# Optimization experiments

Hardware: AMD Instinct MI355X
Metric: run time of the kernel (lower is better)

Reference implementation:

```python
import jax, jax.numpy as jnp
import numpy as np

DN = ('NCHW', 'OIHW', 'NCHW')

def conv(x, w, b, stride, pad):
    y = jax.lax.conv_general_dilated(x, w, (stride, stride), ((pad, pad), (pad, pad)), dimension_numbers=DN)
    return y + b[None, :, None, None]

def conv_transpose(x, w, b, stride, pad):
    # w has torch ConvTranspose2d layout (Cin, Cout, kh, kw)
    k = w.shape[2]
    w_f = jnp.transpose(w[:, :, ::-1, ::-1], (1, 0, 2, 3))  # -> OIHW, spatially flipped
    p = k - 1 - pad
    y = jax.lax.conv_general_dilated(x, w_f, (1, 1), ((p, p), (p, p)), lhs_dilation=(stride, stride), dimension_numbers=DN)
    return y + b[None, :, None, None]

def setup_inputs() -> dict:
    key = jax.random.key(0)
    ks = jax.random.split(key, 16)
    K, D = 512, 64
    s = 0.05
    inp = {
        'x': jax.random.uniform(ks[0], (32, 3, 256, 256), dtype=jnp.float32),
        'enc_w1': jax.random.normal(ks[1], (32, 3, 4, 4), jnp.float32) * s,
        'enc_b1': jnp.zeros((32,), jnp.float32),
        'enc_w2': jax.random.normal(ks[2], (64, 32, 4, 4), jnp.float32) * s,
        'enc_b2': jnp.zeros((64,), jnp.float32),
        'enc_w3': jax.random.normal(ks[3], (D, 64, 3, 3), jnp.float32) * s,
        'enc_b3': jnp.zeros((D,), jnp.float32),
        'codebook': jax.random.uniform(ks[4], (K, D), jnp.float32, -1.0 / K, 1.0 / K),
        'dec_w1': jax.random.normal(ks[5], (D, 64, 4, 4), jnp.float32) * s,   # ConvT (Cin,Cout,k,k)
        'dec_b1': jnp.zeros((64,), jnp.float32),
        'dec_w2': jax.random.normal(ks[6], (64, 32, 4, 4), jnp.float32) * s,  # ConvT
        'dec_b2': jnp.zeros((32,), jnp.float32),
        'dec_w3': jax.random.normal(ks[7], (3, 32, 3, 3), jnp.float32) * s,
        'dec_b3': jnp.zeros((3,), jnp.float32),
    }
    return inp

COMMITMENT_COST = 0.25

def reference(x, enc_w1, enc_b1, enc_w2, enc_b2, enc_w3, enc_b3, codebook,
              dec_w1, dec_b1, dec_w2, dec_b2, dec_w3, dec_b3):
    sg = jax.lax.stop_gradient
    # encoder
    h = jax.nn.relu(conv(x, enc_w1, enc_b1, 2, 1))
    h = jax.nn.relu(conv(h, enc_w2, enc_b2, 2, 1))
    z = conv(h, enc_w3, enc_b3, 1, 1)  # [B, D, H/4, W/4]
    # vector quantizer
    D = codebook.shape[1]
    z_perm = jnp.transpose(z, (0, 2, 3, 1))  # BHWD
    flat = z_perm.reshape(-1, D)  # [N, D]
    dist = jnp.sum(flat * flat, axis=1, keepdims=True) - 2.0 * (flat @ codebook.T) + jnp.sum(codebook * codebook, axis=1)  # [N, K]
    idx = jnp.argmin(dist, axis=1)
    q = codebook[idx].reshape(z_perm.shape)
    q = jnp.transpose(q, (0, 3, 1, 2))  # BDHW
    vq_loss = jnp.mean((sg(q) - z) ** 2) + COMMITMENT_COST * jnp.mean((q - sg(z)) ** 2)
    q_st = z + sg(q - z)  # straight-through
    # decoder
    h = jax.nn.relu(conv_transpose(q_st, dec_w1, dec_b1, 2, 1))
    h = jax.nn.relu(conv_transpose(h, dec_w2, dec_b2, 2, 1))
    recon = jax.nn.sigmoid(conv(h, dec_w3, dec_b3, 1, 1))
    return recon, vq_loss
```

## Files before the change

kernel.cpp:

```cpp
#include <hip/hip_runtime.h>

typedef unsigned short u16;
typedef unsigned int u32;
typedef __attribute__((ext_vector_type(8))) short bf16x8;
typedef __attribute__((ext_vector_type(4))) float f32x4;

#define MFMA(a, b, c) __builtin_amdgcn_mfma_f32_16x16x32_bf16(a, b, c, 0, 0, 0)

__device__ __forceinline__ float b2f(u32 lo16) {
  union { u32 i; float f; } v; v.i = lo16 << 16; return v.f;
}
__device__ __forceinline__ u16 f2b(float f) {
  union { float f; u32 i; } v; v.f = f;
  return (u16)((v.i + 0x7fffu + ((v.i >> 16) & 1u)) >> 16);
}
__device__ __forceinline__ u16 f2bt(float f) {
  union { float f; u32 i; } v; v.f = f;
  return (u16)(v.i >> 16);
}
__device__ __forceinline__ bf16x8 ld8(const u16* p) { return *(const bf16x8*)p; }

__global__ void prep_k(const float* __restrict__ ew1, const float* __restrict__ ew2,
                       const float* __restrict__ ew3, const float* __restrict__ dw1,
                       const float* __restrict__ dw2, const float* __restrict__ dw3,
                       const float* __restrict__ cb,
                       float* W1, u16* Bp2, u16* Bp3, u16* BpT1, u16* BpT2,
                       u16* Bpd3, u16* Bpvq, float* cnorm, float* loss) {
  int tid = blockIdx.x * blockDim.x + threadIdx.x;
  int nth = gridDim.x * blockDim.x;
  for (int i = tid; i < 1536; i += nth) {
    int oc = i & 31; int r = i >> 5; int kw = r & 3; r >>= 2; int kh = r & 3; int ic = r >> 2;
    W1[i] = ew1[((oc*3 + ic)*4 + kh)*4 + kw];
  }
  for (int i = tid; i < 32768; i += nth) {
    int j = i & 7, li = (i >> 3) & 63, nt = (i >> 9) & 3, t = i >> 11;
    int ic = 8*(li >> 4) + j, oc = 16*nt + (li & 15), kh = t >> 2, kw = t & 3;
    Bp2[i] = f2b(ew2[((oc*32 + ic)*4 + kh)*4 + kw]);
  }
  for (int i = tid; i < 36864; i += nth) {
    int j = i & 7, li = (i >> 3) & 63, nt = (i >> 9) & 3, kc = (i >> 11) & 1, t = i >> 12;
    int ic = 32*kc + 8*(li >> 4) + j, oc = 16*nt + (li & 15), kh = t / 3, kw = t % 3;
    Bp3[i] = f2b(ew3[((oc*64 + ic)*3 + kh)*3 + kw]);
  }
  for (int i = tid; i < 65536; i += nth) {
    int j = i & 7, li = (i >> 3) & 63, nt = (i >> 9) & 3, kc = (i >> 11) & 1,
        t = (i >> 12) & 3, p = i >> 14;
    int a = p >> 1, b = p & 1;
    int ky = (1 - a) + 2*(t >> 1), kx = (1 - b) + 2*(t & 1);
    int ic = 32*kc + 8*(li >> 4) + j, oc = 16*nt + (li & 15);
    BpT1[i] = f2b(dw1[((ic*64 + oc)*4 + ky)*4 + kx]);
  }
  for (int i = tid; i < 32768; i += nth) {
    int j = i & 7, li = (i >> 3) & 63, nt = (i >> 9) & 1, kc = (i >> 10) & 1,
        t = (i >> 11) & 3, p = i >> 13;
    int a = p >> 1, b = p & 1;
    int ky = (1 - a) + 2*(t >> 1), kx = (1 - b) + 2*(t & 1);
    int ic = 32*kc + 8*(li >> 4) + j, oc = 16*nt + (li & 15);
    BpT2[i] = f2b(dw2[((ic*32 + oc)*4 + ky)*4 + kx]);
  }
  for (int i = tid; i < 4608; i += nth) {
    int j = i & 7, li = (i >> 3) & 63, t = i >> 9;
    int n = li & 15, ic = 8*(li >> 4) + j, kh = t / 3, kw = t % 3;
    Bpd3[i] = (n < 3) ? f2b(dw3[((n*32 + ic)*3 + kh)*3 + kw]) : (u16)0;
  }
  for (int i = tid; i < 32768; i += nth) {
    int j = i & 7, li = (i >> 3) & 63, nt = (i >> 9) & 31, kc = i >> 14;
    int d = 32*kc + 8*(li >> 4) + j, code = 16*nt + (li & 15);
    Bpvq[i] = f2b(cb[code*64 + d]);
  }
  for (int k = tid; k < 512; k += nth) {
    float s = 0.f;
    for (int d = 0; d < 64; ++d) { float c = cb[k*64 + d]; s += c*c; }
    cnorm[k] = s;
  }
  if (tid == 0) *loss = 0.f;
}

__global__ __launch_bounds__(256) void conv1_k(
    const float* __restrict__ x, const float* __restrict__ W1,
    const float* __restrict__ b1, u16* __restrict__ h1) {
  __shared__ float ins[3*18*36];
  int Tx = blockIdx.x, Ty = blockIdx.y, b = blockIdx.z;
  int tid = threadIdx.x;
  for (int i = tid; i < 3*18*36; i += 256) {
    int c = i % 36; int r = (i / 36) % 18; int ic = i / 648;
    int iy = 16*Ty - 1 + r, ix = 32*Tx - 2 + c;
    float v = 0.f;
    if ((unsigned)iy < 256u && (unsigned)ix < 256u)
      v = x[((size_t)(b*3 + ic)*256 + iy)*256 + ix];
    ins[i] = v;
  }
  __syncthreads();
  int posg = tid & 31, ocg = tid >> 5;
  int Y = posg >> 2, Xg = posg & 3;
  int oc0 = ocg * 4;
  float acc[4][4];
#pragma unroll
  for (int j = 0; j < 4; ++j) { float bv = b1[oc0 + j];
#pragma unroll
    for (int e = 0; e < 4; ++e) acc[j][e] = bv; }
  for (int ic = 0; ic < 3; ++ic)
#pragma unroll
    for (int kh = 0; kh < 4; ++kh) {
      const float* row = &ins[ic*648 + (2*Y + kh)*36 + 8*Xg];
      float win[12];
#pragma unroll
      for (int t = 0; t < 12; ++t) win[t] = row[t];
#pragma unroll
      for (int kw = 0; kw < 4; ++kw) {
        const float* wp = &W1[((ic*4 + kh)*4 + kw)*32 + oc0];
        float w0 = wp[0], w1 = wp[1], w2 = wp[2], w3 = wp[3];
#pragma unroll
        for (int e = 0; e < 4; ++e) {
          float v = win[2*e + kw + 1];
          acc[0][e] += w0*v; acc[1][e] += w1*v; acc[2][e] += w2*v; acc[3][e] += w3*v;
        }
      }
    }
  int oy = 8*Ty + Y;
  int oxb = 16*Tx + 4*Xg;
#pragma unroll
  for (int e = 0; e < 4; ++e) {
    u16* op = &h1[((size_t)(b*128 + oy)*128 + oxb + e)*32 + oc0];
#pragma unroll
    for (int j = 0; j < 4; ++j) op[j] = f2b(fmaxf(acc[j][e], 0.f));
  }
}

__global__ __launch_bounds__(256) void conv2_k(
    const u16* __restrict__ h1, const u16* __restrict__ Bp2,
    const float* __restrict__ eb2, u16* __restrict__ h2) {
  __shared__ u16 lds[2448*8];
  int Tx = blockIdx.x, Ty = blockIdx.y, img = blockIdx.z;
  int tid = threadIdx.x;
  for (int i = tid; i < 2448; i += 256) {
    int c = i & 3; int x = (i >> 2) % 34; int row = (i >> 2) / 34;
    int iy = 16*Ty - 1 + row, ix = 32*Tx - 1 + x;
    f32x4 v = {0,0,0,0};
    if ((unsigned)iy < 128u && (unsigned)ix < 128u)
      v = *(const f32x4*)(h1 + (((size_t)(img*128 + iy)*128 + ix)*32 + c*8));
    *(f32x4*)(lds + ((row*4 + c)*34 + x)*8) = v;
  }
  __syncthreads();
  int w = tid >> 6, l = tid & 63, lg = l >> 4, lc = l & 15;
  f32x4 acc[2][4];
#pragma unroll
  for (int nt = 0; nt < 4; ++nt) {
    float bv = eb2[nt*16 + lc];
    acc[0][nt] = (f32x4){bv,bv,bv,bv}; acc[1][nt] = (f32x4){bv,bv,bv,bv};
  }
#pragma unroll
  for (int t = 0; t < 16; ++t) {
    int kh = t >> 2, kw = t & 3;
    bf16x8 a0 = ld8(lds + (((2*w + kh)*4 + lg)*34 + 2*lc + kw)*8);
    bf16x8 a1 = ld8(lds + (((2*(w+4) + kh)*4 + lg)*34 + 2*lc + kw)*8);
    const u16* bp = Bp2 + t*2048 + l*8;
    bf16x8 b0 = ld8(bp), b1 = ld8(bp + 512), b2v = ld8(bp + 1024), b3v = ld8(bp + 1536);
    acc[0][0] = MFMA(a0, b0, acc[0][0]); acc[0][1] = MFMA(a0, b1, acc[0][1]);
    acc[0][2] = MFMA(a0, b2v, acc[0][2]); acc[0][3] = MFMA(a0, b3v, acc[0][3]);
    acc[1][0] = MFMA(a1, b0, acc[1][0]); acc[1][1] = MFMA(a1, b1, acc[1][1]);
    acc[1][2] = MFMA(a1, b2v, acc[1][2]); acc[1][3] = MFMA(a1, b3v, acc[1][3]);
  }
#pragma unroll
  for (int m = 0; m < 2; ++m) {
    int oy = 8*Ty + w + m*4;
#pragma unroll
    for (int nt = 0; nt < 4; ++nt)
#pragma unroll
      for (int r = 0; r < 4; ++r) {
        int e = 4*lg + r;
        h2[((size_t)(img*64 + oy)*64 + 16*Tx + e)*64 + nt*16 + lc] =
            f2b(fmaxf(acc[m][nt][r], 0.f));
      }
  }
}

__global__ __launch_bounds__(256) void conv3e_k(
    const u16* __restrict__ h2, const u16* __restrict__ Bp3,
    const float* __restrict__ eb3, u16* __restrict__ z) {
  __shared__ u16 lds[1440*8];
  int Tx = blockIdx.x, Ty = blockIdx.y, img = blockIdx.z;
  int tid = threadIdx.x;
  for (int i = tid; i < 1440; i += 256) {
    int c = i & 7; int x = (i >> 3) % 18; int row = (i >> 3) / 18;
    int iy = 8*Ty - 1 + row, ix = 16*Tx - 1 + x;
    f32x4 v = {0,0,0,0};
    if ((unsigned)iy < 64u && (unsigned)ix < 64u)
      v = *(const f32x4*)(h2 + (((size_t)(img*64 + iy)*64 + ix)*64 + c*8));
    *(f32x4*)(lds + ((row*8 + c)*18 + x)*8) = v;
  }
  __syncthreads();
  int w = tid >> 6, l = tid & 63, lg = l >> 4, lc = l & 15;
  f32x4 acc[2][4];
#pragma unroll
  for (int nt = 0; nt < 4; ++nt) {
    float bv = eb3[nt*16 + lc];
    acc[0][nt] = (f32x4){bv,bv,bv,bv}; acc[1][nt] = (f32x4){bv,bv,bv,bv};
  }
#pragma unroll
  for (int t = 0; t < 9; ++t) {
    int kh = t / 3, kw = t % 3;
#pragma unroll
    for (int kc = 0; kc < 2; ++kc) {
      bf16x8 a0 = ld8(lds + (((w + kh)*8 + kc*4 + lg)*18 + lc + kw)*8);
      bf16x8 a1 = ld8(lds + (((w + 4 + kh)*8 + kc*4 + lg)*18 + lc + kw)*8);
      const u16* bp = Bp3 + (t*2 + kc)*2048 + l*8;
      bf16x8 b0 = ld8(bp), b1 = ld8(bp + 512), b2v = ld8(bp + 1024), b3v = ld8(bp + 1536);
      acc[0][0] = MFMA(a0, b0, acc[0][0]); acc[0][1] = MFMA(a0, b1, acc[0][1]);
      acc[0][2] = MFMA(a0, b2v, acc[0][2]); acc[0][3] = MFMA(a0, b3v, acc[0][3]);
      acc[1][0] = MFMA(a1, b0, acc[1][0]); acc[1][1] = MFMA(a1, b1, acc[1][1]);
      acc[1][2] = MFMA(a1, b2v, acc[1][2]); acc[1][3] = MFMA(a1, b3v, acc[1][3]);
    }
  }
#pragma unroll
  for (int m = 0; m < 2; ++m) {
    int oy = 8*Ty + w + m*4;
#pragma unroll
    for (int nt = 0; nt < 4; ++nt)
#pragma unroll
      for (int r = 0; r < 4; ++r) {
        int e = 4*lg + r;
        z[((size_t)(img*64 + oy)*64 + 16*Tx + e)*64 + nt*16 + lc] = f2b(acc[m][nt][r]);
      }
  }
}

__global__ __launch_bounds__(256) void vqm_k(
    const u16* __restrict__ z, const u16* __restrict__ Bpvq,
    const float* __restrict__ cnorm, const float* __restrict__ cbf,
    u16* __restrict__ q, float* __restrict__ loss) {
  __shared__ u16 cbl[32768];
  __shared__ float cnl[512];
  __shared__ int idxl[64];
  __shared__ float red[256];
  int tid = threadIdx.x;
  for (int i = tid; i < 4096; i += 256)
    *(f32x4*)(cbl + i*8) = *(const f32x4*)(Bpvq + i*8);
  for (int i = tid; i < 512; i += 256) cnl[i] = cnorm[i];
  __syncthreads();
  int w = tid >> 6, l = tid & 63, lg = l >> 4, lc = l & 15;
  int wglobal = blockIdx.x*4 + w;
  float lsum = 0.f;
  for (int it = 0; it < 8; ++it) {
    int mf = wglobal + it*1024;
    size_t P = (size_t)mf * 16;
    bf16x8 a0 = ld8(z + (P + lc)*64 + lg*8);
    bf16x8 a1 = ld8(z + (P + lc)*64 + 32 + lg*8);
    float best[4] = {1e30f, 1e30f, 1e30f, 1e30f};
    int bidx[4] = {0, 0, 0, 0};
    for (int nt = 0; nt < 32; ++nt) {
      f32x4 acc = {0,0,0,0};
      acc = MFMA(a0, ld8(cbl + (nt*64 + l)*8), acc);
      acc = MFMA(a1, ld8(cbl + ((32 + nt)*64 + l)*8), acc);
      float cn = cnl[nt*16 + lc];
      int code = nt*16 + lc;
#pragma unroll
      for (int r = 0; r < 4; ++r) {
        float dist = cn - 2.f*acc[r];
        if (dist < best[r]) { best[r] = dist; bidx[r] = code; }
      }
    }
#pragma unroll
    for (int r = 0; r < 4; ++r) {
      float b = best[r]; int bi = bidx[r];
      for (int m = 1; m < 16; m <<= 1) {
        float ob = __shfl_xor(b, m);
        int oi = __shfl_xor(bi, m);
        if (ob < b || (ob == b && oi < bi)) { b = ob; bi = oi; }
      }
      if (lc == 0) idxl[w*16 + lg*4 + r] = bi;
    }
    int m = lc, ch0 = lg*16;
    int id = idxl[w*16 + m];
    const float* crow = cbf + (size_t)id*64 + ch0;
    const u16* zp = z + (P + m)*64 + ch0;
    u32* qp = (u32*)(q + (P + m)*64 + ch0);
#pragma unroll
    for (int c = 0; c < 16; c += 2) {
      float c0 = crow[c], c1 = crow[c+1];
      float d0 = c0 - b2f(zp[c]), d1 = c1 - b2f(zp[c+1]);
      lsum += d0*d0 + d1*d1;
      qp[c >> 1] = (u32)f2bt(c0) | ((u32)f2bt(c1) << 16);
    }
  }
  red[tid] = lsum;
  __syncthreads();
  for (int s = 128; s > 0; s >>= 1) {
    if (tid < s) red[tid] += red[tid + s];
    __syncthreads();
  }
  if (tid == 0) atomicAdd(loss, red[0] * (1.25f / 8388608.f));
}

__global__ __launch_bounds__(256) void convt1_k(
    const u16* __restrict__ q, const u16* __restrict__ BpT1,
    const float* __restrict__ db1, u16* __restrict__ d1) {
  __shared__ u16 lds[864*8];
  int Tx = blockIdx.x, Ty = blockIdx.y, img = blockIdx.z;
  int X0 = 16*Tx, P0 = 4*Ty;
  int tid = threadIdx.x;
  for (int i = tid; i < 864; i += 256) {
    int c = i & 7; int x = (i >> 3) % 18; int row = (i >> 3) / 18;
    int iy = P0 - 1 + row, ix = X0 - 1 + x;
    f32x4 v = {0,0,0,0};
    if ((unsigned)iy < 64u && (unsigned)ix < 64u)
      v = *(const f32x4*)(q + (((size_t)(img*64 + iy)*64 + ix)*64 + c*8));
    *(f32x4*)(lds + ((row*8 + c)*18 + x)*8) = v;
  }
  __syncthreads();
  int w = tid >> 6, l = tid & 63, lg = l >> 4, lc = l & 15;
  int a = w & 1, bp_ = w >> 1;
  f32x4 acc[4][4];
#pragma unroll
  for (int nt = 0; nt < 4; ++nt) {
    float bv = db1[nt*16 + lc];
#pragma unroll
    for (int m = 0; m < 4; ++m) acc[m][nt] = (f32x4){bv,bv,bv,bv};
  }
  const u16* bbase = BpT1 + (size_t)(a*2 + bp_)*16384;
#pragma unroll
  for (int t = 0; t < 4; ++t) {
    int kyi = t >> 1, kxi = t & 1;
#pragma unroll
    for (int kc = 0; kc < 2; ++kc) {
      const u16* bp = bbase + (t*2 + kc)*2048 + l*8;
      bf16x8 b0 = ld8(bp), b1 = ld8(bp + 512), b2v = ld8(bp + 1024), b3v = ld8(bp + 1536);
      int xg = lc + bp_ - kxi + 1;
#pragma unroll
      for (int m = 0; m < 4; ++m) {
        int rowg = m + a - kyi + 1;
        bf16x8 av = ld8(lds + ((rowg*8 + kc*4 + lg)*18 + xg)*8);
        acc[m][0] = MFMA(av, b0, acc[m][0]);
        acc[m][1] = MFMA(av, b1, acc[m][1]);
        acc[m][2] = MFMA(av, b2v, acc[m][2]);
        acc[m][3] = MFMA(av, b3v, acc[m][3]);
      }
    }
  }
#pragma unroll
  for (int m = 0; m < 4; ++m) {
    int oy = 2*(P0 + m) + a;
#pragma unroll
    for (int nt = 0; nt < 4; ++nt)
#pragma unroll
      for (int r = 0; r < 4; ++r) {
        int e = 4*lg + r;
        int ox = 2*(X0 + e) + bp_;
        d1[((size_t)(img*128 + oy)*128 + ox)*64 + nt*16 + lc] =
            f2bt(fmaxf(acc[m][nt][r], 0.f));
      }
  }
}

__global__ __launch_bounds__(256) void tail_k(
    const u16* __restrict__ d1, const u16* __restrict__ BpT2,
    const float* __restrict__ db2, const u16* __restrict__ Bpd3,
    const float* __restrict__ db3, float* __restrict__ out) {
  __shared__ u16 d1s[680*8];
  __shared__ u16 d2q[8192];
  int Tx = blockIdx.x, Ty = blockIdx.y, img = blockIdx.z;
  int DX0 = 30*Tx - 1, DY0 = 6*Ty - 1;
  int IYB = 3*Ty, IXB = 15*Tx;
  int tid = threadIdx.x;
  for (int i = tid; i < 680; i += 256) {
    int x = i % 17; int rc = i / 17; int c = rc & 7; int row = rc >> 3;
    int iy = IYB - 1 + row, ix = IXB - 1 + x;
    f32x4 v = {0,0,0,0};
    if ((unsigned)iy < 128u && (unsigned)ix < 128u)
      v = *(const f32x4*)(d1 + (((size_t)(img*128 + iy)*128 + ix)*64 + c*8));
    *(f32x4*)(d1s + ((row*8 + c)*17 + x)*8) = v;
  }
  __syncthreads();
  int w = tid >> 6, l = tid & 63, lg = l >> 4, lc = l & 15;
  {
    int a = w & 1, b = w >> 1;
    f32x4 acc[4][2];
#pragma unroll
    for (int nt = 0; nt < 2; ++nt) {
      float bv = db2[nt*16 + lc];
#pragma unroll
      for (int m = 0; m < 4; ++m) acc[m][nt] = (f32x4){bv,bv,bv,bv};
    }
    const u16* bbase = BpT2 + (size_t)(a*2 + b)*8192;
#pragma unroll
    for (int kxi = 0; kxi < 2; ++kxi) {
      int xg = lc - kxi + 1;
#pragma unroll
      for (int kc = 0; kc < 2; ++kc) {
        bf16x8 av[5];
#pragma unroll
        for (int rr = 0; rr < 5; ++rr)
          av[rr] = ld8(d1s + ((rr*8 + kc*4 + lg)*17 + xg)*8);
#pragma unroll
        for (int kyi = 0; kyi < 2; ++kyi) {
          int t = kyi*2 + kxi;
          const u16* bb = bbase + (t*2 + kc)*1024 + l*8;
          bf16x8 b0 = ld8(bb), b1 = ld8(bb + 512);
#pragma unroll
          for (int m = 0; m < 4; ++m) {
            acc[m][0] = MFMA(av[m + 1 - kyi], b0, acc[m][0]);
            acc[m][1] = MFMA(av[m + 1 - kyi], b1, acc[m][1]);
          }
        }
      }
    }
    int oyb = DY0 + (1 - a);
    int oxb = DX0 + (1 - b) + 8*lg;
    bool cm[4];
#pragma unroll
    for (int r = 0; r < 4; ++r) cm[r] = (unsigned)(oxb + 2*r) < 256u;
    int base = (a*2 + b)*2048 + lg*128 + lc;
    int ntk = (lg & 1);
#pragma unroll
    for (int m = 0; m < 4; ++m) {
      bool rm = (unsigned)(oyb + 2*m) < 256u;
#pragma unroll
      for (int nt = 0; nt < 2; ++nt) {
        int wb = base + m*512 + ((nt ^ ntk) << 4);
#pragma unroll
        for (int r = 0; r < 4; ++r) {
          float v = (rm && cm[r]) ? fmaxf(acc[m][nt][r], 0.f) : 0.f;
          d2q[wb + r*32] = f2bt(v);
        }
      }
    }
  }
  __syncthreads();
  bf16x8 bw[9];
#pragma unroll
  for (int t = 0; t < 9; ++t) bw[t] = ld8(Bpd3 + t*512 + l*8);
  float bv3 = (lc < 3) ? db3[lc] : 0.f;
#pragma unroll
  for (int i = 0; i < 3; ++i) {
    int u = w + 4*i;
    int yy = u >> 1, xf = u & 1;
    int gy = DY0 + 1 + yy;
    f32x4 acc = {bv3, bv3, bv3, bv3};
#pragma unroll
    for (int t = 0; t < 9; ++t) {
      int kh = t / 3, kw = t % 3;
      int ly = yy + kh;
      int lx = xf*16 + lc + kw;
      if (lx > 31) lx = 31;
      int quad = (1 - (ly & 1))*2 + (1 - (lx & 1));
      int ridx = quad*2048 + (ly >> 1)*512 + (lx >> 1)*32 + ((lg*8) ^ ((lx & 8)*2));
      acc = MFMA(ld8(d2q + ridx), bw[t], acc);
    }
    if (lc < 3 && (unsigned)gy < 256u) {
#pragma unroll
      for (int r = 0; r < 4; ++r) {
        int xi = xf*16 + 4*lg + r;
        int gx = DX0 + 1 + xi;
        if (xi < 30 && (unsigned)gx < 256u)
          out[((size_t)(img*3 + lc)*256 + gy)*256 + gx] = 1.f / (1.f + expf(-acc[r]));
      }
    }
  }
}

extern "C" void kernel_launch(void* const* d_in, const int* in_sizes, int n_in,
                              void* d_out, int out_size, void* d_ws, size_t ws_size,
                              hipStream_t stream) {
  const float* x   = (const float*)d_in[0];
  const float* ew1 = (const float*)d_in[1];
  const float* eb1 = (const float*)d_in[2];
  const float* ew2 = (const float*)d_in[3];
  const float* eb2 = (const float*)d_in[4];
  const float* ew3 = (const float*)d_in[5];
  const float* eb3 = (const float*)d_in[6];
  const float* cb  = (const float*)d_in[7];
  const float* dw1 = (const float*)d_in[8];
  const float* db1 = (const float*)d_in[9];
  const float* dw2 = (const float*)d_in[10];
  const float* db2 = (const float*)d_in[11];
  const float* dw3 = (const float*)d_in[12];
  const float* db3 = (const float*)d_in[13];
  float* out = (float*)d_out;

  char* ws = (char*)d_ws;
  const size_t MB = 1048576;
  u16* h1 = (u16*)ws;
  u16* q  = (u16*)ws;
  u16* d1 = (u16*)(ws + 16*MB);
  u16* h2 = (u16*)(ws + 32*MB);
  u16* z  = (u16*)(ws + 48*MB);
  char* wp = ws + 80*MB;
  float* W1   = (float*)wp;  wp += 6144;
  u16*  Bp2   = (u16*)wp;    wp += 65536;
  u16*  Bp3   = (u16*)wp;    wp += 73728;
  u16*  BpT1  = (u16*)wp;    wp += 131072;
  u16*  BpT2  = (u16*)wp;    wp += 65536;
  u16*  Bpd3  = (u16*)wp;    wp += 9216;
  u16*  Bpvq  = (u16*)wp;    wp += 65536;
  float* cnorm = (float*)wp; wp += 2048;
  float* loss = out + 6291456;

  prep_k<<<64, 256, 0, stream>>>(ew1, ew2, ew3, dw1, dw2, dw3, cb,
                                 W1, Bp2, Bp3, BpT1, BpT2, Bpd3, Bpvq, cnorm, loss);
  conv1_k<<<dim3(8, 16, 32), 256, 0, stream>>>(x, W1, eb1, h1);
  conv2_k<<<dim3(4, 8, 32), 256, 0, stream>>>(h1, Bp2, eb2, h2);
  conv3e_k<<<dim3(4, 8, 32), 256, 0, stream>>>(h2, Bp3, eb3, z);
  vqm_k<<<256, 256, 0, stream>>>(z, Bpvq, cnorm, cb, q, loss);
  convt1_k<<<dim3(4, 16, 32), 256, 0, stream>>>(q, BpT1, db1, d1);
  tail_k<<<dim3(9, 43, 32), 256, 0, stream>>>(d1, BpT2, db2, Bpd3, db3, out);
}
```

Baseline: 290.5 us.

## Shrink conv tiles, widen VQ grid, and restructure tail kernel LDS layout

```diff
diff --git a/kernel.cpp b/kernel.cpp
--- a/kernel.cpp
+++ b/kernel.cpp
@@ -51,11 +51,12 @@
     BpT1[i] = f2b(dw1[((ic*64 + oc)*4 + ky)*4 + kx]);
   }
   for (int i = tid; i < 32768; i += nth) {
-    int j = i & 7, li = (i >> 3) & 63, nt = (i >> 9) & 1, kc = (i >> 10) & 1,
+    int j = i & 7, li = (i >> 3) & 63, mt = (i >> 9) & 1, kc = (i >> 10) & 1,
         t = (i >> 11) & 3, p = i >> 13;
     int a = p >> 1, b = p & 1;
     int ky = (1 - a) + 2*(t >> 1), kx = (1 - b) + 2*(t & 1);
-    int ic = 32*kc + 8*(li >> 4) + j, oc = 16*nt + (li & 15);
+    int oc = 16*mt + (li & 15);
+    int ic = 32*kc + 8*(li >> 4) + j;
     BpT2[i] = f2b(dw2[((ic*32 + oc)*4 + ky)*4 + kx]);
   }
   for (int i = tid; i < 4608; i += nth) {
@@ -130,12 +131,12 @@
 __global__ __launch_bounds__(256) void conv2_k(
     const u16* __restrict__ h1, const u16* __restrict__ Bp2,
     const float* __restrict__ eb2, u16* __restrict__ h2) {
-  __shared__ u16 lds[2448*8];
+  __shared__ u16 lds[1360*8];
   int Tx = blockIdx.x, Ty = blockIdx.y, img = blockIdx.z;
   int tid = threadIdx.x;
-  for (int i = tid; i < 2448; i += 256) {
+  for (int i = tid; i < 1360; i += 256) {
     int c = i & 3; int x = (i >> 2) % 34; int row = (i >> 2) / 34;
-    int iy = 16*Ty - 1 + row, ix = 32*Tx - 1 + x;
+    int iy = 8*Ty - 1 + row, ix = 32*Tx - 1 + x;
     f32x4 v = {0,0,0,0};
     if ((unsigned)iy < 128u && (unsigned)ix < 128u)
       v = *(const f32x4*)(h1 + (((size_t)(img*128 + iy)*128 + ix)*32 + c*8));
@@ -143,47 +144,42 @@
   }
   __syncthreads();
   int w = tid >> 6, l = tid & 63, lg = l >> 4, lc = l & 15;
-  f32x4 acc[2][4];
+  f32x4 acc[4];
 #pragma unroll
   for (int nt = 0; nt < 4; ++nt) {
     float bv = eb2[nt*16 + lc];
-    acc[0][nt] = (f32x4){bv,bv,bv,bv}; acc[1][nt] = (f32x4){bv,bv,bv,bv};
+    acc[nt] = (f32x4){bv,bv,bv,bv};
   }
 #pragma unroll
   for (int t = 0; t < 16; ++t) {
     int kh = t >> 2, kw = t & 3;
     bf16x8 a0 = ld8(lds + (((2*w + kh)*4 + lg)*34 + 2*lc + kw)*8);
-    bf16x8 a1 = ld8(lds + (((2*(w+4) + kh)*4 + lg)*34 + 2*lc + kw)*8);
     const u16* bp = Bp2 + t*2048 + l*8;
-    bf16x8 b0 = ld8(bp), b1 = ld8(bp + 512), b2v = ld8(bp + 1024), b3v = ld8(bp + 1536);
-    acc[0][0] = MFMA(a0, b0, acc[0][0]); acc[0][1] = MFMA(a0, b1, acc[0][1]);
-    acc[0][2] = MFMA(a0, b2v, acc[0][2]); acc[0][3] = MFMA(a0, b3v, acc[0][3]);
-    acc[1][0] = MFMA(a1, b0, acc[1][0]); acc[1][1] = MFMA(a1, b1, acc[1][1]);
-    acc[1][2] = MFMA(a1, b2v, acc[1][2]); acc[1][3] = MFMA(a1, b3v, acc[1][3]);
-  }
-#pragma unroll
-  for (int m = 0; m < 2; ++m) {
-    int oy = 8*Ty + w + m*4;
-#pragma unroll
-    for (int nt = 0; nt < 4; ++nt)
-#pragma unroll
-      for (int r = 0; r < 4; ++r) {
-        int e = 4*lg + r;
-        h2[((size_t)(img*64 + oy)*64 + 16*Tx + e)*64 + nt*16 + lc] =
-            f2b(fmaxf(acc[m][nt][r], 0.f));
-      }
-  }
+    acc[0] = MFMA(a0, ld8(bp), acc[0]);
+    acc[1] = MFMA(a0, ld8(bp + 512), acc[1]);
+    acc[2] = MFMA(a0, ld8(bp + 1024), acc[2]);
+    acc[3] = MFMA(a0, ld8(bp + 1536), acc[3]);
+  }
+  int oy = 4*Ty + w;
+#pragma unroll
+  for (int nt = 0; nt < 4; ++nt)
+#pragma unroll
+    for (int r = 0; r < 4; ++r) {
+      int e = 4*lg + r;
+      h2[((size_t)(img*64 + oy)*64 + 16*Tx + e)*64 + nt*16 + lc] =
+          f2b(fmaxf(acc[nt][r], 0.f));
+    }
 }
 
 __global__ __launch_bounds__(256) void conv3e_k(
     const u16* __restrict__ h2, const u16* __restrict__ Bp3,
     const float* __restrict__ eb3, u16* __restrict__ z) {
-  __shared__ u16 lds[1440*8];
+  __shared__ u16 lds[864*8];
   int Tx = blockIdx.x, Ty = blockIdx.y, img = blockIdx.z;
   int tid = threadIdx.x;
-  for (int i = tid; i < 1440; i += 256) {
+  for (int i = tid; i < 864; i += 256) {
     int c = i & 7; int x = (i >> 3) % 18; int row = (i >> 3) / 18;
-    int iy = 8*Ty - 1 + row, ix = 16*Tx - 1 + x;
+    int iy = 4*Ty - 1 + row, ix = 16*Tx - 1 + x;
     f32x4 v = {0,0,0,0};
     if ((unsigned)iy < 64u && (unsigned)ix < 64u)
       v = *(const f32x4*)(h2 + (((size_t)(img*64 + iy)*64 + ix)*64 + c*8));
@@ -191,11 +187,11 @@
   }
   __syncthreads();
   int w = tid >> 6, l = tid & 63, lg = l >> 4, lc = l & 15;
-  f32x4 acc[2][4];
+  f32x4 acc[4];
 #pragma unroll
   for (int nt = 0; nt < 4; ++nt) {
     float bv = eb3[nt*16 + lc];
-    acc[0][nt] = (f32x4){bv,bv,bv,bv}; acc[1][nt] = (f32x4){bv,bv,bv,bv};
+    acc[nt] = (f32x4){bv,bv,bv,bv};
   }
 #pragma unroll
   for (int t = 0; t < 9; ++t) {
@@ -203,26 +199,21 @@
 #pragma unroll
     for (int kc = 0; kc < 2; ++kc) {
       bf16x8 a0 = ld8(lds + (((w + kh)*8 + kc*4 + lg)*18 + lc + kw)*8);
-      bf16x8 a1 = ld8(lds + (((w + 4 + kh)*8 + kc*4 + lg)*18 + lc + kw)*8);
       const u16* bp = Bp3 + (t*2 + kc)*2048 + l*8;
-      bf16x8 b0 = ld8(bp), b1 = ld8(bp + 512), b2v = ld8(bp + 1024), b3v = ld8(bp + 1536);
-      acc[0][0] = MFMA(a0, b0, acc[0][0]); acc[0][1] = MFMA(a0, b1, acc[0][1]);
-      acc[0][2] = MFMA(a0, b2v, acc[0][2]); acc[0][3] = MFMA(a0, b3v, acc[0][3]);
-      acc[1][0] = MFMA(a1, b0, acc[1][0]); acc[1][1] = MFMA(a1, b1, acc[1][1]);
-      acc[1][2] = MFMA(a1, b2v, acc[1][2]); acc[1][3] = MFMA(a1, b3v, acc[1][3]);
-    }
-  }
-#pragma unroll
-  for (int m = 0; m < 2; ++m) {
-    int oy = 8*Ty + w + m*4;
-#pragma unroll
-    for (int nt = 0; nt < 4; ++nt)
-#pragma unroll
-      for (int r = 0; r < 4; ++r) {
-        int e = 4*lg + r;
-        z[((size_t)(img*64 + oy)*64 + 16*Tx + e)*64 + nt*16 + lc] = f2b(acc[m][nt][r]);
-      }
-  }
+      acc[0] = MFMA(a0, ld8(bp), acc[0]);
+      acc[1] = MFMA(a0, ld8(bp + 512), acc[1]);
+      acc[2] = MFMA(a0, ld8(bp + 1024), acc[2]);
+      acc[3] = MFMA(a0, ld8(bp + 1536), acc[3]);
+    }
+  }
+  int oy = 4*Ty + w;
+#pragma unroll
+  for (int nt = 0; nt < 4; ++nt)
+#pragma unroll
+    for (int r = 0; r < 4; ++r) {
+      int e = 4*lg + r;
+      z[((size_t)(img*64 + oy)*64 + 16*Tx + e)*64 + nt*16 + lc] = f2b(acc[nt][r]);
+    }
 }
 
 __global__ __launch_bounds__(256) void vqm_k(
@@ -241,8 +232,8 @@
   int w = tid >> 6, l = tid & 63, lg = l >> 4, lc = l & 15;
   int wglobal = blockIdx.x*4 + w;
   float lsum = 0.f;
-  for (int it = 0; it < 8; ++it) {
-    int mf = wglobal + it*1024;
+  for (int it = 0; it < 2; ++it) {
+    int mf = wglobal + it*4096;
     size_t P = (size_t)mf * 16;
     bf16x8 a0 = ld8(z + (P + lc)*64 + lg*8);
     bf16x8 a1 = ld8(z + (P + lc)*64 + 32 + lg*8);
@@ -357,11 +348,12 @@
     const float* __restrict__ db2, const u16* __restrict__ Bpd3,
     const float* __restrict__ db3, float* __restrict__ out) {
   __shared__ u16 d1s[680*8];
-  __shared__ u16 d2q[8192];
+  __shared__ u16 d2q[9216];
   int Tx = blockIdx.x, Ty = blockIdx.y, img = blockIdx.z;
   int DX0 = 30*Tx - 1, DY0 = 6*Ty - 1;
   int IYB = 3*Ty, IXB = 15*Tx;
   int tid = threadIdx.x;
+  bool edge = (Tx == 0) | (Tx == 8) | (Ty == 0) | (Ty == 42);
   for (int i = tid; i < 680; i += 256) {
     int x = i % 17; int rc = i / 17; int c = rc & 7; int row = rc >> 3;
     int iy = IYB - 1 + row, ix = IXB - 1 + x;
@@ -376,10 +368,10 @@
     int a = w & 1, b = w >> 1;
     f32x4 acc[4][2];
 #pragma unroll
-    for (int nt = 0; nt < 2; ++nt) {
-      float bv = db2[nt*16 + lc];
-#pragma unroll
-      for (int m = 0; m < 4; ++m) acc[m][nt] = (f32x4){bv,bv,bv,bv};
+    for (int mt = 0; mt < 2; ++mt) {
+      f32x4 bv = *(const f32x4*)(db2 + 16*mt + 4*lg);
+#pragma unroll
+      for (int m = 0; m < 4; ++m) acc[m][mt] = bv;
     }
     const u16* bbase = BpT2 + (size_t)(a*2 + b)*8192;
 #pragma unroll
@@ -394,33 +386,44 @@
 #pragma unroll
         for (int kyi = 0; kyi < 2; ++kyi) {
           int t = kyi*2 + kxi;
-          const u16* bb = bbase + (t*2 + kc)*1024 + l*8;
-          bf16x8 b0 = ld8(bb), b1 = ld8(bb + 512);
+          const u16* wb = bbase + (t*2 + kc)*1024 + l*8;
+          bf16x8 w0 = ld8(wb), w1 = ld8(wb + 512);
 #pragma unroll
           for (int m = 0; m < 4; ++m) {
-            acc[m][0] = MFMA(av[m + 1 - kyi], b0, acc[m][0]);
-            acc[m][1] = MFMA(av[m + 1 - kyi], b1, acc[m][1]);
+            acc[m][0] = MFMA(w0, av[m + 1 - kyi], acc[m][0]);
+            acc[m][1] = MFMA(w1, av[m + 1 - kyi], acc[m][1]);
           }
         }
       }
     }
-    int oyb = DY0 + (1 - a);
-    int oxb = DX0 + (1 - b) + 8*lg;
-    bool cm[4];
-#pragma unroll
-    for (int r = 0; r < 4; ++r) cm[r] = (unsigned)(oxb + 2*r) < 256u;
-    int base = (a*2 + b)*2048 + lg*128 + lc;
-    int ntk = (lg & 1);
-#pragma unroll
-    for (int m = 0; m < 4; ++m) {
-      bool rm = (unsigned)(oyb + 2*m) < 256u;
-#pragma unroll
-      for (int nt = 0; nt < 2; ++nt) {
-        int wb = base + m*512 + ((nt ^ ntk) << 4);
-#pragma unroll
-        for (int r = 0; r < 4; ++r) {
-          float v = (rm && cm[r]) ? fmaxf(acc[m][nt][r], 0.f) : 0.f;
-          d2q[wb + r*32] = f2bt(v);
+    int base = (a*2 + b)*2304 + lc*36 + 4*lg;
+    if (!edge) {
+#pragma unroll
+      for (int m = 0; m < 4; ++m)
+#pragma unroll
+        for (int mt = 0; mt < 2; ++mt) {
+          f32x4 v = acc[m][mt];
+          u32 lo = (u32)f2bt(fmaxf(v[0], 0.f)) | ((u32)f2bt(fmaxf(v[1], 0.f)) << 16);
+          u32 hi = (u32)f2bt(fmaxf(v[2], 0.f)) | ((u32)f2bt(fmaxf(v[3], 0.f)) << 16);
+          *(uint2*)(d2q + base + m*576 + mt*16) = (uint2){lo, hi};
+        }
+    } else {
+      int oxc = b ? DX0 : DX0 + 1;
+      bool cm = (unsigned)(oxc + 2*lc) < 256u;
+      int oyc = a ? DY0 : DY0 + 1;
+#pragma unroll
+      for (int m = 0; m < 4; ++m) {
+        bool rm = (unsigned)(oyc + 2*m) < 256u;
+        bool ok = rm && cm;
+#pragma unroll
+        for (int mt = 0; mt < 2; ++mt) {
+          f32x4 v = acc[m][mt];
+          u32 lo = 0, hi = 0;
+          if (ok) {
+            lo = (u32)f2bt(fmaxf(v[0], 0.f)) | ((u32)f2bt(fmaxf(v[1], 0.f)) << 16);
+            hi = (u32)f2bt(fmaxf(v[2], 0.f)) | ((u32)f2bt(fmaxf(v[3], 0.f)) << 16);
+          }
+          *(uint2*)(d2q + base + m*576 + mt*16) = (uint2){lo, hi};
         }
       }
     }
@@ -435,24 +438,43 @@
     int u = w + 4*i;
     int yy = u >> 1, xf = u & 1;
     int gy = DY0 + 1 + yy;
+    int cOff[3];
+#pragma unroll
+    for (int kw = 0; kw < 3; ++kw) {
+      int lx = xf*16 + lc + kw; if (lx > 31) lx = 31;
+      cOff[kw] = (1 - (lx & 1))*2304 + (lx >> 1)*36 + 8*lg;
+    }
     f32x4 acc = {bv3, bv3, bv3, bv3};
 #pragma unroll
-    for (int t = 0; t < 9; ++t) {
-      int kh = t / 3, kw = t % 3;
+    for (int kh = 0; kh < 3; ++kh) {
       int ly = yy + kh;
-      int lx = xf*16 + lc + kw;
-      if (lx > 31) lx = 31;
-      int quad = (1 - (ly & 1))*2 + (1 - (lx & 1));
-      int ridx = quad*2048 + (ly >> 1)*512 + (lx >> 1)*32 + ((lg*8) ^ ((lx & 8)*2));
-      acc = MFMA(ld8(d2q + ridx), bw[t], acc);
-    }
-    if (lc < 3 && (unsigned)gy < 256u) {
-#pragma unroll
-      for (int r = 0; r < 4; ++r) {
-        int xi = xf*16 + 4*lg + r;
-        int gx = DX0 + 1 + xi;
-        if (xi < 30 && (unsigned)gx < 256u)
-          out[((size_t)(img*3 + lc)*256 + gy)*256 + gx] = 1.f / (1.f + expf(-acc[r]));
+      int rOff = (1 - (ly & 1))*4608 + (ly >> 1)*576;
+#pragma unroll
+      for (int kw = 0; kw < 3; ++kw) {
+        union { bf16x8 v; uint2 u2[2]; } fr;
+        const u16* p = d2q + rOff + cOff[kw];
+        fr.u2[0] = *(const uint2*)p;
+        fr.u2[1] = *(const uint2*)(p + 4);
+        acc = MFMA(fr.v, bw[kh*3 + kw], acc);
+      }
+    }
+    if (lc < 3) {
+      if (!edge) {
+#pragma unroll
+        for (int r = 0; r < 4; ++r) {
+          int xi = xf*16 + 4*lg + r;
+          if (xi < 30)
+            out[((size_t)(img*3 + lc)*256 + gy)*256 + DX0 + 1 + xi] =
+                1.f / (1.f + expf(-acc[r]));
+        }
+      } else if ((unsigned)gy < 256u) {
+#pragma unroll
+        for (int r = 0; r < 4; ++r) {
+          int xi = xf*16 + 4*lg + r;
+          int gx = DX0 + 1 + xi;
+          if (xi < 30 && (unsigned)gx < 256u)
+            out[((size_t)(img*3 + lc)*256 + gy)*256 + gx] = 1.f / (1.f + expf(-acc[r]));
+        }
       }
     }
   }
@@ -498,9 +520,9 @@
   prep_k<<<64, 256, 0, stream>>>(ew1, ew2, ew3, dw1, dw2, dw3, cb,
                                  W1, Bp2, Bp3, BpT1, BpT2, Bpd3, Bpvq, cnorm, loss);
   conv1_k<<<dim3(8, 16, 32), 256, 0, stream>>>(x, W1, eb1, h1);
-  conv2_k<<<dim3(4, 8, 32), 256, 0, stream>>>(h1, Bp2, eb2, h2);
-  conv3e_k<<<dim3(4, 8, 32), 256, 0, stream>>>(h2, Bp3, eb3, z);
-  vqm_k<<<256, 256, 0, stream>>>(z, Bpvq, cnorm, cb, q, loss);
+  conv2_k<<<dim3(4, 16, 32), 256, 0, stream>>>(h1, Bp2, eb2, h2);
+  conv3e_k<<<dim3(4, 16, 32), 256, 0, stream>>>(h2, Bp3, eb3, z);
+  vqm_k<<<1024, 256, 0, stream>>>(z, Bpvq, cnorm, cb, q, loss);
   convt1_k<<<dim3(4, 16, 32), 256, 0, stream>>>(q, BpT1, db1, d1);
   tail_k<<<dim3(9, 43, 32), 256, 0, stream>>>(d1, BpT2, db2, Bpd3, db3, out);
 }
```

Result: slower. 317.6 us (+9.3%).
